# Optimization experiments

Hardware: AMD Instinct MI355X
Metric: run time of the kernel (lower is better)

Reference implementation:

```python
import jax, jax.numpy as jnp
import numpy as np

E = 256        # emb_size
H = 8          # num_heads
D = E // H     # head_dim = 32
FF = 3 * E     # 768
NE = 6         # num_experts
TOPK = 2
EPS = 1e-6


def rotate_half(x):
    x1 = x[..., ::2]
    x2 = x[..., 1::2]
    return jnp.stack((-x2, x1), axis=-1).reshape(x.shape)


def rope_cos_sin(seq_len):
    inv_freq = 1.0 / (10000.0 ** (jnp.arange(0, D, 2, dtype=jnp.float32) / D))
    pos = jnp.arange(seq_len, dtype=jnp.float32)
    freqs = jnp.outer(pos, inv_freq)              # [S, D/2]
    emb = jnp.concatenate([freqs, freqs], axis=-1)  # [S, D]
    return jnp.cos(emb)[None, None], jnp.sin(emb)[None, None]


def rmsnorm(x, w):
    rms = jax.lax.rsqrt(jnp.mean(x * x, axis=-1, keepdims=True) + EPS)
    return x * rms * w


def setup_inputs() -> dict:
    key = jax.random.key(0)
    ks = jax.random.split(key, 10)
    s = lambda fan_in: 1.0 / np.sqrt(fan_in)
    return {
        "x": jax.random.normal(ks[0], (4, 2048, E), dtype=jnp.float32),
        "Wqkv": jax.random.uniform(ks[1], (E, 3 * E), jnp.float32, -s(E), s(E)),
        "Wout": jax.random.uniform(ks[2], (E, E), jnp.float32, -s(E), s(E)),
        "rms1_w": jnp.ones((E,), jnp.float32),
        "rms2_w": jnp.ones((E,), jnp.float32),
        "gate_W": jax.random.uniform(ks[3], (E, NE), jnp.float32, -s(E), s(E)),
        "Wg": jax.random.uniform(ks[4], (NE, E, FF), jnp.float32, -s(E), s(E)),
        "Wu": jax.random.uniform(ks[5], (NE, E, FF), jnp.float32, -s(E), s(E)),
        "Wd": jax.random.uniform(ks[6], (NE, FF, E), jnp.float32, -s(FF), s(FF)),
    }


def attention(xn, Wqkv, Wout):
    B, S, _ = xn.shape
    qkv = (xn @ Wqkv).reshape(B, S, 3, H, D).transpose(2, 0, 3, 1, 4)  # [3,B,H,S,D]
    q, k, v = qkv[0], qkv[1], qkv[2]
    cos, sin = rope_cos_sin(S)
    q = q * cos + rotate_half(q) * sin
    k = k * cos + rotate_half(k) * sin
    scores = jnp.einsum("bhqd,bhkd->bhqk", q, k) * (D ** -0.5)
    causal = jnp.arange(S)[None, :] > jnp.arange(S)[:, None]
    scores = jnp.where(causal[None, None], -jnp.inf, scores)
    attn = jax.nn.softmax(scores, axis=-1)
    out = jnp.einsum("bhqk,bhkd->bhqd", attn, v)
    out = out.transpose(0, 2, 1, 3).reshape(B, S, E)
    return out @ Wout


def moe(xn, gate_W, Wg, Wu, Wd):
    B, S, _ = xn.shape
    N = B * S
    gate_weights = jax.nn.softmax(xn @ gate_W, axis=-1)          # [B,S,NE]
    topk_w, topk_i = jax.lax.top_k(gate_weights, TOPK)           # [B,S,K]
    topk_w = jax.nn.softmax(topk_w, axis=-1)
    xf = xn.reshape(N, E)
    idx = topk_i.reshape(N, TOPK)
    wts = topk_w.reshape(N, TOPK)
    # dense all-expert compute, as in the original
    expert_out = jnp.einsum("ntf,nfe->nte",
                            jax.nn.silu(jnp.einsum("te,nef->ntf", xf, Wg))
                            * jnp.einsum("te,nef->ntf", xf, Wu),
                            Wd)                                   # [NE, N, E]
    weighted_sel = jnp.zeros((N, NE), xf.dtype).at[jnp.arange(N)[:, None], idx].add(wts)
    out = jnp.einsum("nte,tn->te", expert_out, weighted_sel).reshape(B, S, E)
    # load balancing aux loss
    importance = gate_weights.mean(axis=(0, 1))                   # [NE]
    load = jnp.zeros((NE,), xf.dtype).at[idx.reshape(-1)].add(1.0) / N
    aux_loss = NE * jnp.sum(importance * load)
    return out, aux_loss


def reference(x, Wqkv, Wout, rms1_w, rms2_w, gate_W, Wg, Wu, Wd):
    attn_out = attention(rmsnorm(x, rms1_w), Wqkv, Wout)
    x = x + attn_out
    ff_out, aux_loss = moe(rmsnorm(x, rms2_w), gate_W, Wg, Wu, Wd)
    return x + ff_out, aux_loss
```

## Files before the change

### kernel.cpp

```cpp
#include <hip/hip_runtime.h>
#include <hip/hip_bf16.h>
#include <math.h>

#define NE 6

typedef __bf16 bf16x8 __attribute__((ext_vector_type(8)));
typedef float f32x4 __attribute__((ext_vector_type(4)));
typedef short short8 __attribute__((ext_vector_type(8)));

#define SWZ(row, kbyte) (((row) * 128) + ((kbyte) ^ (((row) & 7) << 4)))

static __device__ __forceinline__ short f2bf(float f) {
    __hip_bfloat16 h = __float2bfloat16(f);
    return __builtin_bit_cast(short, h);
}

static __device__ __forceinline__ float bf2f(short s) {
    return __bfloat162float(__builtin_bit_cast(__hip_bfloat16, s));
}

__global__ void rope_tables(float* __restrict__ ct, float* __restrict__ st) {
    int id = blockIdx.x * 256 + threadIdx.x;
    if (id >= 2048 * 16) return;
    int s = id >> 4, f = id & 15;
    float invf = expf(-logf(10000.0f) * (float)f / 16.0f);
    float ang = (float)s * invf;
    ct[id] = cosf(ang);
    st[id] = sinf(ang);
}

__global__ void rmsnorm_k(const float* __restrict__ x, const float* __restrict__ w,
                          float* __restrict__ o) {
    __shared__ float red[256];
    int n = blockIdx.x, t = threadIdx.x;
    float v = x[n * 256 + t];
    red[t] = v * v;
    __syncthreads();
    for (int s = 128; s > 0; s >>= 1) {
        if (t < s) red[t] += red[t + s];
        __syncthreads();
    }
    float rms = rsqrtf(red[0] / 256.0f + 1e-6f);
    o[n * 256 + t] = v * rms * w[t];
}

__global__ void rmsnorm_both(const float* __restrict__ x, const float* __restrict__ w,
                             float* __restrict__ o, short* __restrict__ obf) {
    __shared__ float red[256];
    int n = blockIdx.x, t = threadIdx.x;
    float v = x[n * 256 + t];
    red[t] = v * v;
    __syncthreads();
    for (int s = 128; s > 0; s >>= 1) {
        if (t < s) red[t] += red[t + s];
        __syncthreads();
    }
    float rms = rsqrtf(red[0] / 256.0f + 1e-6f);
    float val = v * rms * w[t];
    o[n * 256 + t] = val;
    obf[n * 256 + t] = f2bf(val);
}

__global__ __launch_bounds__(256) void transcvt_k(const float* __restrict__ src,
                                                  short* __restrict__ dst, int R, int C) {
    __shared__ short tile[32][33];
    const float* s = src + (size_t)blockIdx.z * R * C;
    short* d = dst + (size_t)blockIdx.z * R * C;
    int t = threadIdx.x;
    int c0 = blockIdx.x * 32, r0 = blockIdx.y * 32;
    int ci = t & 31, ri0 = t >> 5;
#pragma unroll
    for (int it = 0; it < 4; it++) {
        int ri = ri0 + it * 8;
        tile[ri][ci] = f2bf(s[(size_t)(r0 + ri) * C + c0 + ci]);
    }
    __syncthreads();
#pragma unroll
    for (int it = 0; it < 4; it++) {
        int rj = ri0 + it * 8;
        d[(size_t)(c0 + rj) * R + r0 + ci] = tile[ci][rj];
    }
}

__global__ __launch_bounds__(256) void gemm_qkv(const float* __restrict__ A,
                                                const float* __restrict__ W,
                                                float* __restrict__ Q, float* __restrict__ Kq,
                                                float* __restrict__ V) {
    __shared__ float As[16][64];
    __shared__ float Bs[16][64];
    int t = threadIdx.x;
    int m0 = blockIdx.y * 64, n0 = blockIdx.x * 64;
    float acc[4][4] = {};
    int am = t >> 2, ak = (t & 3) * 4;
    int bk = t >> 4, bn = (t & 15) * 4;
    int tm = (t & 15) * 4, tn = (t >> 4) * 4;
    for (int k0 = 0; k0 < 256; k0 += 16) {
        float4 av = *(const float4*)&A[(m0 + am) * 256 + k0 + ak];
        As[ak + 0][am] = av.x; As[ak + 1][am] = av.y; As[ak + 2][am] = av.z; As[ak + 3][am] = av.w;
        float4 bv = *(const float4*)&W[(k0 + bk) * 768 + n0 + bn];
        *(float4*)&Bs[bk][bn] = bv;
        __syncthreads();
#pragma unroll
        for (int kk = 0; kk < 16; kk++) {
            float4 a4 = *(float4*)&As[kk][tm];
            float4 b4 = *(float4*)&Bs[kk][tn];
            float a[4] = {a4.x, a4.y, a4.z, a4.w};
            float b[4] = {b4.x, b4.y, b4.z, b4.w};
#pragma unroll
            for (int i = 0; i < 4; i++)
#pragma unroll
                for (int j = 0; j < 4; j++) acc[i][j] += a[i] * b[j];
        }
        __syncthreads();
    }
    int part = n0 >> 8;
    float* dst = part == 0 ? Q : (part == 1 ? Kq : V);
#pragma unroll
    for (int i = 0; i < 4; i++) {
        int rowi = m0 + tm + i;
        int b = rowi >> 11, s = rowi & 2047;
#pragma unroll
        for (int j = 0; j < 4; j++) {
            int c = n0 + tn + j;
            int e = c & 255, h = e >> 5, d = e & 31;
            dst[(((size_t)(b * 8 + h)) * 2048 + s) * 32 + d] = acc[i][j];
        }
    }
}

__global__ void rope_k(float* __restrict__ Q, float* __restrict__ Kq,
                       const float* __restrict__ ct, const float* __restrict__ st) {
    int id = blockIdx.x * 256 + threadIdx.x;
    if (id >= 32 * 2048 * 16) return;
    int i = id & 15;
    int s = (id >> 4) & 2047;
    int bh = id >> 15;
    int base = (bh * 2048 + s) * 32 + 2 * i;
    int j0 = (2 * i) & 15;
    float c0 = ct[s * 16 + j0], s0 = st[s * 16 + j0];
    float c1 = ct[s * 16 + j0 + 1], s1 = st[s * 16 + j0 + 1];
    float2 q = *(float2*)&Q[base];
    float2 k = *(float2*)&Kq[base];
    float2 qo, ko;
    qo.x = q.x * c0 - q.y * s0;
    qo.y = q.y * c1 + q.x * s1;
    ko.x = k.x * c0 - k.y * s0;
    ko.y = k.y * c1 + k.x * s1;
    *(float2*)&Q[base] = qo;
    *(float2*)&Kq[base] = ko;
}

__global__ __launch_bounds__(256) void attn_k(const float* __restrict__ Q,
                                              const float* __restrict__ Kg,
                                              const float* __restrict__ Vg,
                                              float* __restrict__ ctx) {
    __shared__ float4 Kl[64][8];
    __shared__ float4 Vl[64][8];
    int bh = blockIdx.x;
    int qt = gridDim.y - 1 - blockIdx.y;
    int t = threadIdx.x;
    int sub = t & 3;
    int row = qt * 64 + (t >> 2);
    const float4* Qb = (const float4*)(Q + (size_t)bh * 2048 * 32);
    const float4* Kb = (const float4*)(Kg + (size_t)bh * 2048 * 32);
    const float4* Vb = (const float4*)(Vg + (size_t)bh * 2048 * 32);
    float4 q0 = Qb[row * 8 + sub * 2];
    float4 q1 = Qb[row * 8 + sub * 2 + 1];
    float4 o0 = {}, o1 = {};
    float m = -1e30f, l = 0.f;
    const float scale = 0.17677669529663687f;
    int ntile = qt + 1;
    float4* Klf = &Kl[0][0];
    float4* Vlf = &Vl[0][0];
    for (int kt = 0; kt < ntile; kt++) {
        int kbase = kt * 64;
        Klf[t] = Kb[kbase * 8 + t];
        Klf[t + 256] = Kb[kbase * 8 + t + 256];
        Vlf[t] = Vb[kbase * 8 + t];
        Vlf[t + 256] = Vb[kbase * 8 + t + 256];
        __syncthreads();
        int jmax = row - kbase + 1;
        if (jmax > 64) jmax = 64;
        for (int j = 0; j < jmax; j++) {
            float4 k0 = Kl[j][sub * 2];
            float4 k1 = Kl[j][sub * 2 + 1];
            float s = q0.x * k0.x + q0.y * k0.y + q0.z * k0.z + q0.w * k0.w +
                      q1.x * k1.x + q1.y * k1.y + q1.z * k1.z + q1.w * k1.w;
            s += __shfl_xor(s, 1);
            s += __shfl_xor(s, 2);
            s *= scale;
            if (s > m) {
                float r = __expf(m - s);
                o0.x *= r; o0.y *= r; o0.z *= r; o0.w *= r;
                o1.x *= r; o1.y *= r; o1.z *= r; o1.w *= r;
                l *= r;
                m = s;
            }
            float p = __expf(s - m);
            l += p;
            float4 v0 = Vl[j][sub * 2];
            float4 v1 = Vl[j][sub * 2 + 1];
            o0.x += p * v0.x; o0.y += p * v0.y; o0.z += p * v0.z; o0.w += p * v0.w;
            o1.x += p * v1.x; o1.y += p * v1.y; o1.z += p * v1.z; o1.w += p * v1.w;
        }
        __syncthreads();
    }
    float invl = 1.f / l;
    int b = bh >> 3, h = bh & 7;
    float4* cp = (float4*)(ctx + ((size_t)(b * 2048 + row)) * 256 + h * 32 + sub * 8);
    o0.x *= invl; o0.y *= invl; o0.z *= invl; o0.w *= invl;
    o1.x *= invl; o1.y *= invl; o1.z *= invl; o1.w *= invl;
    cp[0] = o0;
    cp[1] = o1;
}

__global__ __launch_bounds__(256) void gemm_out(const float* __restrict__ A,
                                                const float* __restrict__ W,
                                                const float* __restrict__ xres,
                                                float* __restrict__ x2) {
    __shared__ float As[16][64];
    __shared__ float Bs[16][64];
    int t = threadIdx.x;
    int m0 = blockIdx.y * 64, n0 = blockIdx.x * 64;
    float acc[4][4] = {};
    int am = t >> 2, ak = (t & 3) * 4;
    int bk = t >> 4, bn = (t & 15) * 4;
    int tm = (t & 15) * 4, tn = (t >> 4) * 4;
    for (int k0 = 0; k0 < 256; k0 += 16) {
        float4 av = *(const float4*)&A[(m0 + am) * 256 + k0 + ak];
        As[ak + 0][am] = av.x; As[ak + 1][am] = av.y; As[ak + 2][am] = av.z; As[ak + 3][am] = av.w;
        float4 bv = *(const float4*)&W[(k0 + bk) * 256 + n0 + bn];
        *(float4*)&Bs[bk][bn] = bv;
        __syncthreads();
#pragma unroll
        for (int kk = 0; kk < 16; kk++) {
            float4 a4 = *(float4*)&As[kk][tm];
            float4 b4 = *(float4*)&Bs[kk][tn];
            float a[4] = {a4.x, a4.y, a4.z, a4.w};
            float b[4] = {b4.x, b4.y, b4.z, b4.w};
#pragma unroll
            for (int i = 0; i < 4; i++)
#pragma unroll
                for (int j = 0; j < 4; j++) acc[i][j] += a[i] * b[j];
        }
        __syncthreads();
    }
#pragma unroll
    for (int i = 0; i < 4; i++) {
        int rowi = m0 + tm + i;
#pragma unroll
        for (int j = 0; j < 4; j++) {
            int c = n0 + tn + j;
            x2[rowi * 256 + c] = acc[i][j] + xres[rowi * 256 + c];
        }
    }
}

__global__ void gate_k(const float* __restrict__ xn2, const float* __restrict__ gw,
                       int* __restrict__ idx, float* __restrict__ wts,
                       int* __restrict__ cnt, float* __restrict__ imp) {
    __shared__ float simp[NE];
    __shared__ int scnt[NE];
    int t = threadIdx.x;
    int n = blockIdx.x * 256 + t;
    if (t < NE) { simp[t] = 0.f; scnt[t] = 0; }
    __syncthreads();
    float lg[NE] = {0, 0, 0, 0, 0, 0};
    for (int k = 0; k < 256; k++) {
        float xv = xn2[n * 256 + k];
#pragma unroll
        for (int e = 0; e < NE; e++) lg[e] += xv * gw[k * NE + e];
    }
    float mx = lg[0];
#pragma unroll
    for (int e = 1; e < NE; e++) mx = fmaxf(mx, lg[e]);
    float p[NE], se = 0.f;
#pragma unroll
    for (int e = 0; e < NE; e++) { p[e] = expf(lg[e] - mx); se += p[e]; }
    float inv = 1.f / se;
#pragma unroll
    for (int e = 0; e < NE; e++) p[e] *= inv;
    int i1 = 0; float v1 = p[0];
#pragma unroll
    for (int e = 1; e < NE; e++) if (p[e] > v1) { v1 = p[e]; i1 = e; }
    int i2 = -1; float v2 = -1.f;
#pragma unroll
    for (int e = 0; e < NE; e++) if (e != i1 && p[e] > v2) { v2 = p[e]; i2 = e; }
    float e2v = expf(v2 - v1);
    float w1 = 1.f / (1.f + e2v);
    float w2 = e2v / (1.f + e2v);
    idx[n * 2] = i1; idx[n * 2 + 1] = i2;
    wts[n * 2] = w1; wts[n * 2 + 1] = w2;
#pragma unroll
    for (int e = 0; e < NE; e++) atomicAdd(&simp[e], p[e]);
    atomicAdd(&scnt[i1], 1);
    atomicAdd(&scnt[i2], 1);
    __syncthreads();
    if (t < NE) {
        atomicAdd(&imp[t], simp[t]);
        atomicAdd(&cnt[t], scnt[t]);
    }
}

__global__ void prefix_k(const int* __restrict__ cnt, const float* __restrict__ imp,
                         int* __restrict__ offs, int* __restrict__ cur,
                         float* __restrict__ auxout) {
    if (threadIdx.x == 0) {
        int o = 0;
        float a = 0.f;
        for (int e = 0; e < NE; e++) {
            offs[e] = o;
            cur[e] = o;
            o += cnt[e];
            a += imp[e] * (float)cnt[e];
        }
        auxout[0] = 6.0f * a / (8192.0f * 8192.0f);
    }
}

__global__ void scatter_k(const int* __restrict__ idx, int* __restrict__ cur,
                          int* __restrict__ ltok, int* __restrict__ slotp) {
    int n = blockIdx.x * 256 + threadIdx.x;
#pragma unroll
    for (int s = 0; s < 2; s++) {
        int e = idx[n * 2 + s];
        int pos = atomicAdd(&cur[e], 1);
        ltok[pos] = n;
        slotp[n * 2 + s] = pos;
    }
}

__global__ __launch_bounds__(256) void mfma_moe1(const short* __restrict__ xnbf,
                                                 const short* __restrict__ WgT,
                                                 const short* __restrict__ WuT,
                                                 const int* __restrict__ cnt,
                                                 const int* __restrict__ offs,
                                                 const int* __restrict__ ltok,
                                                 short* __restrict__ Hbuf) {
    int e = blockIdx.z;
    int Me = cnt[e];
    int m0 = blockIdx.y * 64;
    if (m0 >= Me) return;
    int off = offs[e];
    __shared__ short As[4096], Bg[4096], Bu[4096];
    __shared__ int stok[64];
    int t = threadIdx.x;
    if (t < 64) stok[t] = (m0 + t < Me) ? ltok[off + m0 + t] : ltok[off];
    __syncthreads();
    int n0 = blockIdx.x * 64;
    const short* WgE = WgT + (size_t)e * 768 * 256;
    const short* WuE = WuT + (size_t)e * 768 * 256;
    int lane = t & 63, wid = t >> 6, wr = wid >> 1, wc = wid & 1;
    int l15 = lane & 15, lh = lane >> 4;
    int r = t >> 3, k8 = (t & 7) * 8, kb8 = (t & 7) * 16;
    char* AsC = (char*)As; char* BgC = (char*)Bg; char* BuC = (char*)Bu;
    f32x4 accg[2][2] = {}, accu[2][2] = {};
    for (int k0 = 0; k0 < 256; k0 += 64) {
        short8 av0 = *(const short8*)&xnbf[(size_t)stok[r] * 256 + k0 + k8];
        short8 av1 = *(const short8*)&xnbf[(size_t)stok[r + 32] * 256 + k0 + k8];
        short8 gv0 = *(const short8*)&WgE[(size_t)(n0 + r) * 256 + k0 + k8];
        short8 gv1 = *(const short8*)&WgE[(size_t)(n0 + r + 32) * 256 + k0 + k8];
        short8 uv0 = *(const short8*)&WuE[(size_t)(n0 + r) * 256 + k0 + k8];
        short8 uv1 = *(const short8*)&WuE[(size_t)(n0 + r + 32) * 256 + k0 + k8];
        *(short8*)(AsC + SWZ(r, kb8)) = av0;
        *(short8*)(AsC + SWZ(r + 32, kb8)) = av1;
        *(short8*)(BgC + SWZ(r, kb8)) = gv0;
        *(short8*)(BgC + SWZ(r + 32, kb8)) = gv1;
        *(short8*)(BuC + SWZ(r, kb8)) = uv0;
        *(short8*)(BuC + SWZ(r + 32, kb8)) = uv1;
        __syncthreads();
#pragma unroll
        for (int kk = 0; kk < 2; kk++) {
            int kb = kk * 64 + lh * 16;
            bf16x8 a[2], bg[2], bu[2];
#pragma unroll
            for (int i = 0; i < 2; i++) {
                a[i]  = *(const bf16x8*)(AsC + SWZ(wr * 32 + i * 16 + l15, kb));
                bg[i] = *(const bf16x8*)(BgC + SWZ(wc * 32 + i * 16 + l15, kb));
                bu[i] = *(const bf16x8*)(BuC + SWZ(wc * 32 + i * 16 + l15, kb));
            }
#pragma unroll
            for (int mi = 0; mi < 2; mi++)
#pragma unroll
                for (int ni = 0; ni < 2; ni++) {
                    accg[mi][ni] = __builtin_amdgcn_mfma_f32_16x16x32_bf16(a[mi], bg[ni], accg[mi][ni], 0, 0, 0);
                    accu[mi][ni] = __builtin_amdgcn_mfma_f32_16x16x32_bf16(a[mi], bu[ni], accu[mi][ni], 0, 0, 0);
                }
        }
        __syncthreads();
    }
#pragma unroll
    for (int mi = 0; mi < 2; mi++)
#pragma unroll
        for (int j = 0; j < 4; j++) {
            int m = m0 + wr * 32 + mi * 16 + lh * 4 + j;
            if (m < Me) {
                size_t rp = (size_t)(off + m) * 768;
#pragma unroll
                for (int ni = 0; ni < 2; ni++) {
                    int c = n0 + wc * 32 + ni * 16 + l15;
                    float g = accg[mi][ni][j], u = accu[mi][ni][j];
                    Hbuf[rp + c] = f2bf(g / (1.f + __expf(-g)) * u);
                }
            }
        }
}

__global__ __launch_bounds__(256) void mfma_moe2(const short* __restrict__ Hbuf,
                                                 const short* __restrict__ WdT,
                                                 const int* __restrict__ cnt,
                                                 const int* __restrict__ offs,
                                                 short* __restrict__ Y) {
    int e = blockIdx.z;
    int Me = cnt[e];
    int m0 = blockIdx.y * 64;
    if (m0 >= Me) return;
    int off = offs[e];
    __shared__ short As[4096], Bs[4096];
    int t = threadIdx.x;
    int n0 = blockIdx.x * 64;
    const short* WdE = WdT + (size_t)e * 256 * 768;
    int lane = t & 63, wid = t >> 6, wr = wid >> 1, wc = wid & 1;
    int l15 = lane & 15, lh = lane >> 4;
    int r = t >> 3, k8 = (t & 7) * 8, kb8 = (t & 7) * 16;
    int ar0 = off + m0 + r;       if (ar0 > 16383) ar0 = 16383;
    int ar1 = off + m0 + r + 32;  if (ar1 > 16383) ar1 = 16383;
    char* AsC = (char*)As; char* BsC = (char*)Bs;
    f32x4 acc[2][2] = {};
    for (int k0 = 0; k0 < 768; k0 += 64) {
        short8 av0 = *(const short8*)&Hbuf[(size_t)ar0 * 768 + k0 + k8];
        short8 av1 = *(const short8*)&Hbuf[(size_t)ar1 * 768 + k0 + k8];
        short8 bv0 = *(const short8*)&WdE[(size_t)(n0 + r) * 768 + k0 + k8];
        short8 bv1 = *(const short8*)&WdE[(size_t)(n0 + r + 32) * 768 + k0 + k8];
        *(short8*)(AsC + SWZ(r, kb8)) = av0;
        *(short8*)(AsC + SWZ(r + 32, kb8)) = av1;
        *(short8*)(BsC + SWZ(r, kb8)) = bv0;
        *(short8*)(BsC + SWZ(r + 32, kb8)) = bv1;
        __syncthreads();
#pragma unroll
        for (int kk = 0; kk < 2; kk++) {
            int kb = kk * 64 + lh * 16;
            bf16x8 a[2], b[2];
#pragma unroll
            for (int i = 0; i < 2; i++) {
                a[i] = *(const bf16x8*)(AsC + SWZ(wr * 32 + i * 16 + l15, kb));
                b[i] = *(const bf16x8*)(BsC + SWZ(wc * 32 + i * 16 + l15, kb));
            }
#pragma unroll
            for (int mi = 0; mi < 2; mi++)
#pragma unroll
                for (int ni = 0; ni < 2; ni++)
                    acc[mi][ni] = __builtin_amdgcn_mfma_f32_16x16x32_bf16(a[mi], b[ni], acc[mi][ni], 0, 0, 0);
        }
        __syncthreads();
    }
#pragma unroll
    for (int mi = 0; mi < 2; mi++)
#pragma unroll
        for (int j = 0; j < 4; j++) {
            int m = m0 + wr * 32 + mi * 16 + lh * 4 + j;
            if (m < Me) {
                size_t rp = (size_t)(off + m) * 256;
#pragma unroll
                for (int ni = 0; ni < 2; ni++) {
                    int c = n0 + wc * 32 + ni * 16 + l15;
                    Y[rp + c] = f2bf(acc[mi][ni][j]);
                }
            }
        }
}

__global__ void combine_k(const float* __restrict__ x2, const short* __restrict__ Y,
                          const int* __restrict__ slotp, const float* __restrict__ wts,
                          float* __restrict__ out) {
    int n = blockIdx.x, t = threadIdx.x;
    int p0 = slotp[n * 2], p1 = slotp[n * 2 + 1];
    float w0 = wts[n * 2], w1 = wts[n * 2 + 1];
    out[n * 256 + t] = x2[n * 256 + t] + w0 * bf2f(Y[(size_t)p0 * 256 + t]) +
                       w1 * bf2f(Y[(size_t)p1 * 256 + t]);
}

extern "C" void kernel_launch(void* const* d_in, const int* in_sizes, int n_in,
                              void* d_out, int out_size, void* d_ws, size_t ws_size,
                              hipStream_t stream) {
    const float* x     = (const float*)d_in[0];
    const float* Wqkv  = (const float*)d_in[1];
    const float* Wout  = (const float*)d_in[2];
    const float* rms1w = (const float*)d_in[3];
    const float* rms2w = (const float*)d_in[4];
    const float* gateW = (const float*)d_in[5];
    const float* Wg    = (const float*)d_in[6];
    const float* Wu    = (const float*)d_in[7];
    const float* Wd    = (const float*)d_in[8];
    float* out = (float*)d_out;
    char* ws = (char*)d_ws;

    float* xn1   = (float*)(ws + 0);
    short* xn2bf = (short*)(ws + 0);
    float* Qb  = (float*)(ws + 8388608);
    float* Kb  = (float*)(ws + 16777216);
    float* Vb  = (float*)(ws + 25165824);
    short* Hbuf = (short*)(ws + 4194304);
    float* ctx = (float*)(ws + 33554432);
    short* WgT = (short*)(ws + 33554432);
    short* WuT = (short*)(ws + 35913728);
    short* WdT = (short*)(ws + 38273024);
    float* x2  = (float*)(ws + 41943040);
    float* xn2 = (float*)(ws + 50331648);
    short* Ybuf = (short*)(ws + 50331648);
    float* ct  = (float*)(ws + 58720256);
    float* st  = (float*)(ws + 58851328);
    int*   idx = (int*)(ws + 58982400);
    float* wts = (float*)(ws + 59047936);
    int* slotp = (int*)(ws + 59113472);
    int* ltok  = (int*)(ws + 59179008);
    int* cnt   = (int*)(ws + 59244544);
    int* offs  = cnt + 8;
    int* cur   = cnt + 16;
    float* imp = (float*)(cnt + 24);

    (void)hipMemsetAsync(cnt, 0, 128, stream);

    rope_tables<<<128, 256, 0, stream>>>(ct, st);
    rmsnorm_k<<<8192, 256, 0, stream>>>(x, rms1w, xn1);
    gemm_qkv<<<dim3(12, 128), 256, 0, stream>>>(xn1, Wqkv, Qb, Kb, Vb);
    rope_k<<<4096, 256, 0, stream>>>(Qb, Kb, ct, st);
    attn_k<<<dim3(32, 32), 256, 0, stream>>>(Qb, Kb, Vb, ctx);
    gemm_out<<<dim3(4, 128), 256, 0, stream>>>(ctx, Wout, x, x2);
    transcvt_k<<<dim3(24, 8, NE), 256, 0, stream>>>(Wg, WgT, 256, 768);
    transcvt_k<<<dim3(24, 8, NE), 256, 0, stream>>>(Wu, WuT, 256, 768);
    transcvt_k<<<dim3(8, 24, NE), 256, 0, stream>>>(Wd, WdT, 768, 256);
    rmsnorm_both<<<8192, 256, 0, stream>>>(x2, rms2w, xn2, xn2bf);
    gate_k<<<32, 256, 0, stream>>>(xn2, gateW, idx, wts, cnt, imp);
    prefix_k<<<1, 64, 0, stream>>>(cnt, imp, offs, cur, out + 2097152);
    scatter_k<<<32, 256, 0, stream>>>(idx, cur, ltok, slotp);
    mfma_moe1<<<dim3(12, 256, NE), 256, 0, stream>>>(xn2bf, WgT, WuT, cnt, offs, ltok, Hbuf);
    mfma_moe2<<<dim3(4, 256, NE), 256, 0, stream>>>(Hbuf, WdT, cnt, offs, Ybuf);
    combine_k<<<8192, 256, 0, stream>>>(x2, Ybuf, slotp, wts, out);
}
```

Before: 736.0 us.

## Process two query rows per thread in attention to reuse K/V tiles

Each attention block now handles 128 query rows instead of 64: every thread keeps two query rows with separate online-softmax state and reuses each K/V element read from LDS for both. The inner loop also prefetches the next K/V row into registers. The aim is to halve the K/V global loads and LDS reads per query and to overlap LDS latency with compute. The cost is more registers per thread, half as many blocks in the grid, and some wasted work where the first row has already reached its causal limit.

```diff
diff --git a/kernel.cpp b/kernel.cpp
--- a/kernel.cpp
+++ b/kernel.cpp
@@ -160,16 +160,19 @@
     int qt = gridDim.y - 1 - blockIdx.y;
     int t = threadIdx.x;
     int sub = t & 3;
-    int row = qt * 64 + (t >> 2);
+    int row0 = qt * 128 + (t >> 2);
+    int row1 = row0 + 64;
     const float4* Qb = (const float4*)(Q + (size_t)bh * 2048 * 32);
     const float4* Kb = (const float4*)(Kg + (size_t)bh * 2048 * 32);
     const float4* Vb = (const float4*)(Vg + (size_t)bh * 2048 * 32);
-    float4 q0 = Qb[row * 8 + sub * 2];
-    float4 q1 = Qb[row * 8 + sub * 2 + 1];
-    float4 o0 = {}, o1 = {};
-    float m = -1e30f, l = 0.f;
+    float4 qa0 = Qb[row0 * 8 + sub * 2];
+    float4 qa1 = Qb[row0 * 8 + sub * 2 + 1];
+    float4 qb0 = Qb[row1 * 8 + sub * 2];
+    float4 qb1 = Qb[row1 * 8 + sub * 2 + 1];
+    float4 oa0 = {}, oa1 = {}, ob0 = {}, ob1 = {};
+    float ma = -1e30f, la = 0.f, mb = -1e30f, lb = 0.f;
     const float scale = 0.17677669529663687f;
-    int ntile = qt + 1;
+    int ntile = qt * 2 + 2;
     float4* Klf = &Kl[0][0];
     float4* Vlf = &Vl[0][0];
     for (int kt = 0; kt < ntile; kt++) {
@@ -179,39 +182,68 @@
         Vlf[t] = Vb[kbase * 8 + t];
         Vlf[t + 256] = Vb[kbase * 8 + t + 256];
         __syncthreads();
-        int jmax = row - kbase + 1;
-        if (jmax > 64) jmax = 64;
-        for (int j = 0; j < jmax; j++) {
-            float4 k0 = Kl[j][sub * 2];
-            float4 k1 = Kl[j][sub * 2 + 1];
-            float s = q0.x * k0.x + q0.y * k0.y + q0.z * k0.z + q0.w * k0.w +
-                      q1.x * k1.x + q1.y * k1.y + q1.z * k1.z + q1.w * k1.w;
-            s += __shfl_xor(s, 1);
-            s += __shfl_xor(s, 2);
-            s *= scale;
-            if (s > m) {
-                float r = __expf(m - s);
-                o0.x *= r; o0.y *= r; o0.z *= r; o0.w *= r;
-                o1.x *= r; o1.y *= r; o1.z *= r; o1.w *= r;
-                l *= r;
-                m = s;
+        int ja = row0 - kbase + 1;
+        if (ja > 64) ja = 64;
+        if (ja < 0) ja = 0;
+        int jb = row1 - kbase + 1;
+        if (jb > 64) jb = 64;
+        float4 k0 = Kl[0][sub * 2], k1 = Kl[0][sub * 2 + 1];
+        float4 v0 = Vl[0][sub * 2], v1 = Vl[0][sub * 2 + 1];
+        for (int j = 0; j < jb; j++) {
+            int jn = (j + 1 < 64) ? j + 1 : 63;
+            float4 nk0 = Kl[jn][sub * 2], nk1 = Kl[jn][sub * 2 + 1];
+            float4 nv0 = Vl[jn][sub * 2], nv1 = Vl[jn][sub * 2 + 1];
+            float sA = qa0.x * k0.x + qa0.y * k0.y + qa0.z * k0.z + qa0.w * k0.w +
+                       qa1.x * k1.x + qa1.y * k1.y + qa1.z * k1.z + qa1.w * k1.w;
+            float sB = qb0.x * k0.x + qb0.y * k0.y + qb0.z * k0.z + qb0.w * k0.w +
+                       qb1.x * k1.x + qb1.y * k1.y + qb1.z * k1.z + qb1.w * k1.w;
+            sA += __shfl_xor(sA, 1);
+            sA += __shfl_xor(sA, 2);
+            sB += __shfl_xor(sB, 1);
+            sB += __shfl_xor(sB, 2);
+            sA *= scale;
+            sB *= scale;
+            if (j < ja) {
+                if (sA > ma) {
+                    float r = __expf(ma - sA);
+                    oa0.x *= r; oa0.y *= r; oa0.z *= r; oa0.w *= r;
+                    oa1.x *= r; oa1.y *= r; oa1.z *= r; oa1.w *= r;
+                    la *= r;
+                    ma = sA;
+                }
+                float p = __expf(sA - ma);
+                la += p;
+                oa0.x += p * v0.x; oa0.y += p * v0.y; oa0.z += p * v0.z; oa0.w += p * v0.w;
+                oa1.x += p * v1.x; oa1.y += p * v1.y; oa1.z += p * v1.z; oa1.w += p * v1.w;
             }
-            float p = __expf(s - m);
-            l += p;
-            float4 v0 = Vl[j][sub * 2];
-            float4 v1 = Vl[j][sub * 2 + 1];
-            o0.x += p * v0.x; o0.y += p * v0.y; o0.z += p * v0.z; o0.w += p * v0.w;
-            o1.x += p * v1.x; o1.y += p * v1.y; o1.z += p * v1.z; o1.w += p * v1.w;
-        }
-        __syncthreads();
-    }
-    float invl = 1.f / l;
+            if (sB > mb) {
+                float r = __expf(mb - sB);
+                ob0.x *= r; ob0.y *= r; ob0.z *= r; ob0.w *= r;
+                ob1.x *= r; ob1.y *= r; ob1.z *= r; ob1.w *= r;
+                lb *= r;
+                mb = sB;
+            }
+            float pB = __expf(sB - mb);
+            lb += pB;
+            ob0.x += pB * v0.x; ob0.y += pB * v0.y; ob0.z += pB * v0.z; ob0.w += pB * v0.w;
+            ob1.x += pB * v1.x; ob1.y += pB * v1.y; ob1.z += pB * v1.z; ob1.w += pB * v1.w;
+            k0 = nk0; k1 = nk1; v0 = nv0; v1 = nv1;
+        }
+        __syncthreads();
+    }
     int b = bh >> 3, h = bh & 7;
-    float4* cp = (float4*)(ctx + ((size_t)(b * 2048 + row)) * 256 + h * 32 + sub * 8);
-    o0.x *= invl; o0.y *= invl; o0.z *= invl; o0.w *= invl;
-    o1.x *= invl; o1.y *= invl; o1.z *= invl; o1.w *= invl;
-    cp[0] = o0;
-    cp[1] = o1;
+    float invla = 1.f / la;
+    float4* cpa = (float4*)(ctx + ((size_t)(b * 2048 + row0)) * 256 + h * 32 + sub * 8);
+    oa0.x *= invla; oa0.y *= invla; oa0.z *= invla; oa0.w *= invla;
+    oa1.x *= invla; oa1.y *= invla; oa1.z *= invla; oa1.w *= invla;
+    cpa[0] = oa0;
+    cpa[1] = oa1;
+    float invlb = 1.f / lb;
+    float4* cpb = (float4*)(ctx + ((size_t)(b * 2048 + row1)) * 256 + h * 32 + sub * 8);
+    ob0.x *= invlb; ob0.y *= invlb; ob0.z *= invlb; ob0.w *= invlb;
+    ob1.x *= invlb; ob1.y *= invlb; ob1.z *= invlb; ob1.w *= invlb;
+    cpb[0] = ob0;
+    cpb[1] = ob1;
 }
 
 __global__ __launch_bounds__(256) void gemm_out(const float* __restrict__ A,
@@ -525,7 +557,7 @@
     rmsnorm_k<<<8192, 256, 0, stream>>>(x, rms1w, xn1);
     gemm_qkv<<<dim3(12, 128), 256, 0, stream>>>(xn1, Wqkv, Qb, Kb, Vb);
     rope_k<<<4096, 256, 0, stream>>>(Qb, Kb, ct, st);
-    attn_k<<<dim3(32, 32), 256, 0, stream>>>(Qb, Kb, Vb, ctx);
+    attn_k<<<dim3(32, 16), 256, 0, stream>>>(Qb, Kb, Vb, ctx);
     gemm_out<<<dim3(4, 128), 256, 0, stream>>>(ctx, Wout, x, x2);
     transcvt_k<<<dim3(24, 8, NE), 256, 0, stream>>>(Wg, WgT, 256, 768);
     transcvt_k<<<dim3(24, 8, NE), 256, 0, stream>>>(Wu, WuT, 256, 768);
```

After: 829.2 us. +12.7%, slower.
